# Optimization experiments

Measured on AMD Instinct MI355X. Metric: run time of the kernel, lower is better.

The kernel has to match this reference:

```python
import jax, jax.numpy as jnp
import numpy as np

N_ENTS = 100000
N_EDGES = 200000
H = 256
NUM_RELS = 200  # embedding table has 2*NUM_RELS rows
TYPE_DIM = H // 4


def layer_norm(x, g, b, eps=1e-5):
    m = jnp.mean(x, axis=-1, keepdims=True)
    v = jnp.var(x, axis=-1, keepdims=True)
    return (x - m) * jax.lax.rsqrt(v + eps) * g + b


def setup_inputs() -> dict:
    key = jax.random.key(0)
    ks = jax.random.split(key, 20)
    s = 0.02  # xavier-ish scale for weights
    return {
        "node_emb": jax.random.normal(ks[0], (N_ENTS, H), jnp.float32),
        "h_prev": jax.random.normal(ks[1], (N_ENTS, H), jnp.float32),
        "type_emb": jax.random.normal(ks[2], (2 * NUM_RELS, TYPE_DIM), jnp.float32) * s,
        "W_edge": jax.random.normal(ks[3], (2 * H + TYPE_DIM, H), jnp.float32) * s,
        "b_edge": jnp.zeros((H,), jnp.float32),
        "ln_edge_g": jnp.ones((H,), jnp.float32),
        "ln_edge_b": jnp.zeros((H,), jnp.float32),
        "W_gate": jax.random.normal(ks[4], (2 * H, H), jnp.float32) * s,
        "b_gate": jnp.zeros((H,), jnp.float32),
        "ln_gate_g": jnp.ones((H,), jnp.float32),
        "ln_gate_b": jnp.zeros((H,), jnp.float32),
        "W_ih": jax.random.normal(ks[5], (3 * H, H), jnp.float32) * s,
        "W_hh": jax.random.normal(ks[6], (3 * H, H), jnp.float32) * s,
        "b_ih": jnp.zeros((3 * H,), jnp.float32),
        "b_hh": jnp.zeros((3 * H,), jnp.float32),
        "ln_gru_g": jnp.ones((H,), jnp.float32),
        "ln_gru_b": jnp.zeros((H,), jnp.float32),
        "src": jax.random.randint(ks[7], (N_EDGES,), 0, N_ENTS, jnp.int32),
        "dst": jax.random.randint(ks[8], (N_EDGES,), 0, N_ENTS, jnp.int32),
        "edge_types": jax.random.randint(ks[9], (N_EDGES,), 0, 2 * NUM_RELS, jnp.int32),
    }


def reference(node_emb, h_prev, type_emb, W_edge, b_edge, ln_edge_g, ln_edge_b,
              W_gate, b_gate, ln_gate_g, ln_gate_b,
              W_ih, W_hh, b_ih, b_hh, ln_gru_g, ln_gru_b,
              src, dst, edge_types):
    # --- EdgeFeatureExtractor: gather + edge MLP (dropout=eval identity) ---
    edge_in = jnp.concatenate(
        [node_emb[src], node_emb[dst], type_emb[edge_types]], axis=1)  # [E, 2H+H/4]
    edge_feat = jax.nn.relu(
        layer_norm(edge_in @ W_edge + b_edge, ln_edge_g, ln_edge_b))  # [E, H]

    # --- create_edge_enhanced_nodes: scatter-mean over dst ---
    agg = jax.ops.segment_sum(edge_feat, dst, num_segments=N_ENTS)  # [N, H]
    cnt = jax.ops.segment_sum(jnp.ones((edge_feat.shape[0],), edge_feat.dtype),
                              dst, num_segments=N_ENTS)
    edge_enh = agg / jnp.clip(cnt, 1.0)[:, None]

    # --- DualStreamProcessor fusion ---
    gate = jax.nn.sigmoid(layer_norm(
        jnp.concatenate([node_emb, edge_enh], axis=1) @ W_gate + b_gate,
        ln_gate_g, ln_gate_b))
    fused = gate * node_emb + (1.0 - gate) * edge_enh
    x = 0.2 * node_emb + 0.8 * fused

    # --- EnhancedGRUCell: torch GRUCell + LayerNorm + 0.3*h residual ---
    gi = x @ W_ih.T + b_ih      # [N, 3H]
    gh = h_prev @ W_hh.T + b_hh  # [N, 3H]
    gi_r, gi_z, gi_n = jnp.split(gi, 3, axis=1)
    gh_r, gh_z, gh_n = jnp.split(gh, 3, axis=1)
    r = jax.nn.sigmoid(gi_r + gh_r)
    z = jax.nn.sigmoid(gi_z + gh_z)
    n = jnp.tanh(gi_n + r * gh_n)
    h = (1.0 - z) * n + z * h_prev
    h = layer_norm(h, ln_gru_g, ln_gru_b) + 0.3 * h_prev
    return h
```

## Files before the change

kernel.cpp:

```cpp
#include <hip/hip_runtime.h>
#include <hip/hip_bf16.h>
#include <hip/hip_fp16.h>

#define H 256
#define TYPE_DIM 64
#define EIN (2*H + TYPE_DIM)
#define N_ENTS 100000
#define N_EDGES 200000
#define EPB 32
#define NPB 64
#define KE 576
#define LDE 584
#define LDF 260
#define LDA 520
#define LDH 264
#define LDF2 260

typedef __hip_bfloat16 bf16;
typedef short bf16x8 __attribute__((ext_vector_type(8)));
typedef float f32x4 __attribute__((ext_vector_type(4)));

__device__ __forceinline__ unsigned short f2b(float f) {
    union { float f; unsigned int u; } v; v.f = f;
    unsigned int u = v.u;
    return (unsigned short)((u + 0x7FFFu + ((u >> 16) & 1u)) >> 16);
}
__device__ __forceinline__ unsigned int pack2(float a, float b) {
    return (unsigned int)f2b(a) | ((unsigned int)f2b(b) << 16);
}
__device__ __forceinline__ float u2f(unsigned short u) {
    union { unsigned int i; float f; } t; t.i = ((unsigned int)u) << 16; return t.f;
}
__device__ __forceinline__ float sigm(float x) { return 1.0f / (1.0f + __expf(-x)); }

__device__ __forceinline__ void atomic_pk_f16(void* p, unsigned int v) {
    asm volatile("global_atomic_pk_add_f16 %0, %1, off" :: "v"(p), "v"(v) : "memory");
}

__device__ __forceinline__ bf16x8 cvt8(const float* p) {
    f32x4 a = *(const f32x4*)p;
    f32x4 b = *(const f32x4*)(p + 4);
    union { bf16 h[8]; bf16x8 v; } u;
    u.h[0] = __float2bfloat16(a[0]); u.h[1] = __float2bfloat16(a[1]);
    u.h[2] = __float2bfloat16(a[2]); u.h[3] = __float2bfloat16(a[3]);
    u.h[4] = __float2bfloat16(b[0]); u.h[5] = __float2bfloat16(b[1]);
    u.h[6] = __float2bfloat16(b[2]); u.h[7] = __float2bfloat16(b[3]);
    return u.v;
}

__global__ void transpose_we(const float* __restrict__ W,
                             unsigned short* __restrict__ WE) {
    int c = blockIdx.x;
    for (int j = threadIdx.x; j < KE; j += 256)
        WE[(size_t)c * KE + j] = f2b(W[(size_t)j * H + c]);
}

__global__ void transpose_wg(const float* __restrict__ W,
                             unsigned short* __restrict__ WG) {
    int c = blockIdx.x;
    for (int k = threadIdx.x; k < 2 * H; k += 256)
        WG[(size_t)c * (2 * H) + k] = f2b(W[(size_t)k * H + c]);
}

__global__ void cast_gru(const float* __restrict__ Wih, const float* __restrict__ Whh,
                         unsigned short* __restrict__ WTih,
                         unsigned short* __restrict__ WThh, int do_hh) {
    int j = blockIdx.x;
    int k = threadIdx.x;
    WTih[(size_t)j * H + k] = f2b(Wih[(size_t)j * H + k]);
    if (do_hh) WThh[(size_t)j * H + k] = f2b(Whh[(size_t)j * H + k]);
}

__global__ __launch_bounds__(256) void edge_mfma(
    const float* __restrict__ node_emb, const float* __restrict__ type_emb,
    const unsigned short* __restrict__ WE,
    const float* __restrict__ b_edge,
    const float* __restrict__ ln_g, const float* __restrict__ ln_b,
    const int* __restrict__ src, const int* __restrict__ dst,
    const int* __restrict__ et,
    unsigned char* __restrict__ aggb,
    unsigned int* __restrict__ cntw) {
    __shared__ __align__(16) unsigned short ein[EPB * LDE];
    __shared__ int sidx[EPB], didx[EPB], tidx[EPB];

    const int tid = threadIdx.x;
    const int e0 = blockIdx.x * EPB;
    const int lane = tid & 63;
    const int w = tid >> 6;
    const int l15 = lane & 15;
    const int l4 = lane >> 4;

    if (tid < EPB) {
        sidx[tid] = src[e0 + tid];
        didx[tid] = dst[e0 + tid];
        tidx[tid] = et[e0 + tid];
    }
    __syncthreads();

    {
        const int half = tid >> 7;
        const int tt = tid & 127;
        #pragma unroll 4
        for (int e = 0; e < EPB; e++) {
            const int n = half ? didx[e] : sidx[e];
            const float2 v = *(const float2*)(node_emb + (size_t)n * H + 2 * tt);
            *(unsigned int*)&ein[e * LDE + half * 256 + 2 * tt] = pack2(v.x, v.y);
        }
        #pragma unroll
        for (int i = tid; i < EPB * 32; i += 256) {
            const int e = i >> 5, j = i & 31;
            const float2 v = *(const float2*)(type_emb + (size_t)tidx[e] * TYPE_DIM + 2 * j);
            *(unsigned int*)&ein[e * LDE + 512 + 2 * j] = pack2(v.x, v.y);
        }
    }
    __syncthreads();

    f32x4 acc[2][4];
    #pragma unroll
    for (int mt = 0; mt < 2; mt++)
        #pragma unroll
        for (int nt = 0; nt < 4; nt++)
            acc[mt][nt] = (f32x4){0.f, 0.f, 0.f, 0.f};

    const int colbase = w * 64;
    const unsigned short* A0 = &ein[l15 * LDE + l4 * 8];
    const unsigned short* A1 = &ein[(16 + l15) * LDE + l4 * 8];
    const unsigned short* B0 = WE + (size_t)(colbase + l15) * KE + l4 * 8;
    const unsigned short* B1 = B0 + 16 * KE;
    const unsigned short* B2 = B0 + 32 * KE;
    const unsigned short* B3 = B0 + 48 * KE;

    for (int ks = 0; ks < KE / 32; ks++) {
        const int o = ks * 32;
        bf16x8 a0 = __builtin_bit_cast(bf16x8, *(const uint4*)(A0 + o));
        bf16x8 a1 = __builtin_bit_cast(bf16x8, *(const uint4*)(A1 + o));
        bf16x8 b0 = __builtin_bit_cast(bf16x8, *(const uint4*)(B0 + o));
        bf16x8 b1 = __builtin_bit_cast(bf16x8, *(const uint4*)(B1 + o));
        bf16x8 b2 = __builtin_bit_cast(bf16x8, *(const uint4*)(B2 + o));
        bf16x8 b3 = __builtin_bit_cast(bf16x8, *(const uint4*)(B3 + o));
        acc[0][0] = __builtin_amdgcn_mfma_f32_16x16x32_bf16(a0, b0, acc[0][0], 0, 0, 0);
        acc[0][1] = __builtin_amdgcn_mfma_f32_16x16x32_bf16(a0, b1, acc[0][1], 0, 0, 0);
        acc[0][2] = __builtin_amdgcn_mfma_f32_16x16x32_bf16(a0, b2, acc[0][2], 0, 0, 0);
        acc[0][3] = __builtin_amdgcn_mfma_f32_16x16x32_bf16(a0, b3, acc[0][3], 0, 0, 0);
        acc[1][0] = __builtin_amdgcn_mfma_f32_16x16x32_bf16(a1, b0, acc[1][0], 0, 0, 0);
        acc[1][1] = __builtin_amdgcn_mfma_f32_16x16x32_bf16(a1, b1, acc[1][1], 0, 0, 0);
        acc[1][2] = __builtin_amdgcn_mfma_f32_16x16x32_bf16(a1, b2, acc[1][2], 0, 0, 0);
        acc[1][3] = __builtin_amdgcn_mfma_f32_16x16x32_bf16(a1, b3, acc[1][3], 0, 0, 0);
    }

    __syncthreads();
    float* fout = (float*)&ein[0];

    float bias[4];
    #pragma unroll
    for (int nt = 0; nt < 4; nt++) bias[nt] = b_edge[colbase + nt * 16 + l15];
    #pragma unroll
    for (int mt = 0; mt < 2; mt++)
        #pragma unroll
        for (int nt = 0; nt < 4; nt++)
            #pragma unroll
            for (int r = 0; r < 4; r++) {
                int row = mt * 16 + l4 * 4 + r;
                fout[row * LDF + colbase + nt * 16 + l15] = acc[mt][nt][r] + bias[nt];
            }
    __syncthreads();

    const float4 gv = *(const float4*)(ln_g + 4 * lane);
    const float4 bv = *(const float4*)(ln_b + 4 * lane);
    for (int rr = 0; rr < 8; rr++) {
        const int row = w * 8 + rr;
        f32x4 v = *(const f32x4*)&fout[row * LDF + 4 * lane];
        float s1 = v[0] + v[1] + v[2] + v[3];
        float s2 = v[0] * v[0] + v[1] * v[1] + v[2] * v[2] + v[3] * v[3];
        #pragma unroll
        for (int o = 32; o > 0; o >>= 1) {
            s1 += __shfl_down(s1, o, 64);
            s2 += __shfl_down(s2, o, 64);
        }
        const float m = __shfl(s1, 0, 64) * (1.0f / (float)H);
        const float q = __shfl(s2, 0, 64) * (1.0f / (float)H);
        const float is = rsqrtf(fmaxf(q - m * m, 0.0f) + 1e-5f);
        float y0 = fmaxf((v[0] - m) * is * gv.x + bv.x, 0.0f);
        float y1 = fmaxf((v[1] - m) * is * gv.y + bv.y, 0.0f);
        float y2 = fmaxf((v[2] - m) * is * gv.z + bv.z, 0.0f);
        float y3 = fmaxf((v[3] - m) * is * gv.w + bv.w, 0.0f);
        __half2 h01 = __floats2half2_rn(y0, y1);
        __half2 h23 = __floats2half2_rn(y2, y3);
        unsigned char* dp = aggb + (size_t)didx[row] * 1024 + lane * 8;
        atomic_pk_f16(dp,     __builtin_bit_cast(unsigned int, h01));
        atomic_pk_f16(dp + 4, __builtin_bit_cast(unsigned int, h23));
    }
    if (tid < EPB) {
        int d = didx[tid];
        atomicAdd(&cntw[d >> 2], 1u << ((d & 3) * 8));
    }
}

template<bool SHH>
__global__ __launch_bounds__(1024, 4) void node_mfma(
    const float* __restrict__ node_emb, const float* __restrict__ h_prev,
    const unsigned short* __restrict__ WG, const float* __restrict__ b_gate,
    const float* __restrict__ lng_g, const float* __restrict__ lng_b,
    const unsigned short* __restrict__ WTih, const unsigned short* __restrict__ WThh,
    const float* __restrict__ Whh_f32,
    const float* __restrict__ b_ih, const float* __restrict__ b_hh,
    const float* __restrict__ lnr_g, const float* __restrict__ lnr_b,
    const unsigned int* __restrict__ cntw,
    float* __restrict__ out) {
    __shared__ __align__(16) unsigned short Aga[NPB * LDA];
    __shared__ __align__(16) unsigned short shr[NPB * LDH];
    __shared__ float rc[NPB];

    const int tid = threadIdx.x;
    const int n0 = blockIdx.x * NPB;
    const int lane = tid & 63;
    const int w = tid >> 6;
    const int l15 = lane & 15, l4 = lane >> 4;

    if (tid < NPB) {
        int n = n0 + tid;
        float c = 1.0f;
        if (n < N_ENTS) {
            unsigned int cw = cntw[n >> 2];
            c = (float)((cw >> ((n & 3) * 8)) & 0xFFu);
        }
        rc[tid] = 1.0f / fmaxf(c, 1.0f);
    }
    __syncthreads();

    const unsigned char* aggb = (const unsigned char*)out;

    for (int i = tid; i < NPB * 128; i += 1024) {
        int row = i >> 7, c2 = (i & 127) * 2;
        int nr = n0 + row;
        size_t gn = (size_t)(nr < N_ENTS ? nr : 0);
        float2 xv = *(const float2*)(node_emb + gn * H + c2);
        unsigned int eu = *(const unsigned int*)(aggb + gn * 1024 + c2 * 2);
        float2 ev = __half22float2(__builtin_bit_cast(__half2, eu));
        float r = rc[row];
        *(unsigned int*)&Aga[row * LDA + c2]       = pack2(xv.x, xv.y);
        *(unsigned int*)&Aga[row * LDA + 256 + c2] = pack2(ev.x * r, ev.y * r);
    }
    __syncthreads();

    {
        f32x4 acc[4];
        #pragma unroll
        for (int m = 0; m < 4; m++) acc[m] = (f32x4){0.f, 0.f, 0.f, 0.f};
        const unsigned short* Ab = &Aga[l15 * LDA + l4 * 8];
        const unsigned short* B0 = WG + (size_t)(w * 16 + l15) * (2 * H) + l4 * 8;
        #pragma unroll 4
        for (int ks = 0; ks < 16; ks++) {
            const int o = ks * 32;
            bf16x8 b0 = __builtin_bit_cast(bf16x8, *(const uint4*)(B0 + o));
            #pragma unroll
            for (int m = 0; m < 4; m++) {
                bf16x8 a = __builtin_bit_cast(bf16x8, *(const uint4*)(Ab + m * 16 * LDA + o));
                acc[m] = __builtin_amdgcn_mfma_f32_16x16x32_bf16(a, b0, acc[m], 0, 0, 0);
            }
        }
        const float bg0 = b_gate[w * 16 + l15];
        #pragma unroll
        for (int m = 0; m < 4; m++)
            #pragma unroll
            for (int r = 0; r < 4; r++) {
                int row = m * 16 + l4 * 4 + r;
                shr[row * LDH + w * 16 + l15] = f2b(acc[m][r] + bg0);
            }
    }
    __syncthreads();

    {
        const float4 g4 = *(const float4*)(lng_g + 4 * lane);
        const float4 b4 = *(const float4*)(lng_b + 4 * lane);
        for (int rr = 0; rr < 4; rr++) {
            const int row = w * 4 + rr;
            short4 us = *(const short4*)&shr[row * LDH + 4 * lane];
            float u0 = u2f((unsigned short)us.x), u1 = u2f((unsigned short)us.y);
            float u2 = u2f((unsigned short)us.z), u3 = u2f((unsigned short)us.w);
            float s1 = u0 + u1 + u2 + u3;
            float s2 = u0 * u0 + u1 * u1 + u2 * u2 + u3 * u3;
            #pragma unroll
            for (int o = 32; o > 0; o >>= 1) {
                s1 += __shfl_down(s1, o, 64);
                s2 += __shfl_down(s2, o, 64);
            }
            const float m = __shfl(s1, 0, 64) * (1.0f / (float)H);
            const float q = __shfl(s2, 0, 64) * (1.0f / (float)H);
            const float is = rsqrtf(fmaxf(q - m * m, 0.0f) + 1e-5f);
            short4 xr = *(const short4*)&Aga[row * LDA + 4 * lane];
            short4 er = *(const short4*)&Aga[row * LDA + 256 + 4 * lane];
            float xv[4] = {u2f((unsigned short)xr.x), u2f((unsigned short)xr.y),
                           u2f((unsigned short)xr.z), u2f((unsigned short)xr.w)};
            float ev[4] = {u2f((unsigned short)er.x), u2f((unsigned short)er.y),
                           u2f((unsigned short)er.z), u2f((unsigned short)er.w)};
            float uu[4] = {u0, u1, u2, u3};
            float gl[4] = {g4.x, g4.y, g4.z, g4.w};
            float bl[4] = {b4.x, b4.y, b4.z, b4.w};
            unsigned short xs[4];
            #pragma unroll
            for (int j = 0; j < 4; j++) {
                float gate = sigm((uu[j] - m) * is * gl[j] + bl[j]);
                float fused = gate * xv[j] + (1.0f - gate) * ev[j];
                xs[j] = f2b(0.2f * xv[j] + 0.8f * fused);
            }
            *(unsigned int*)&Aga[row * LDA + 4 * lane]     = (unsigned int)xs[0] | ((unsigned int)xs[1] << 16);
            *(unsigned int*)&Aga[row * LDA + 4 * lane + 2] = (unsigned int)xs[2] | ((unsigned int)xs[3] << 16);
        }
    }
    __syncthreads();

    for (int i = tid; i < NPB * 128; i += 1024) {
        int row = i >> 7, c2 = (i & 127) * 2;
        int nr = n0 + row;
        size_t g = (size_t)(nr < N_ENTS ? nr : 0) * H + c2;
        float2 hv = *(const float2*)(h_prev + g);
        *(unsigned int*)&shr[row * LDH + c2] = pack2(hv.x, hv.y);
    }
    __syncthreads();

    const int cl = w * 16 + l15;
    const unsigned short* Xb = &Aga[l15 * LDA + l4 * 8];
    const unsigned short* Pb = &shr[l15 * LDH + l4 * 8];

    float rg[4][4], zg[4][4];
    {
        f32x4 aIr[4], aIz[4], aHr[4], aHz[4];
        #pragma unroll
        for (int m = 0; m < 4; m++) {
            aIr[m] = (f32x4){0.f, 0.f, 0.f, 0.f}; aIz[m] = (f32x4){0.f, 0.f, 0.f, 0.f};
            aHr[m] = (f32x4){0.f, 0.f, 0.f, 0.f}; aHz[m] = (f32x4){0.f, 0.f, 0.f, 0.f};
        }
        const unsigned short* bi0 = WTih + (size_t)(cl) * H + l4 * 8;
        const unsigned short* bi1 = WTih + (size_t)(H + cl) * H + l4 * 8;
        const unsigned short* bh0s = WThh + (size_t)(cl) * H + l4 * 8;
        const unsigned short* bh1s = WThh + (size_t)(H + cl) * H + l4 * 8;
        const float* fh0 = Whh_f32 + (size_t)(cl) * H + l4 * 8;
        const float* fh1 = Whh_f32 + (size_t)(H + cl) * H + l4 * 8;
        #pragma unroll 4
        for (int ks = 0; ks < 8; ks++) {
            const int o = ks * 32;
            bf16x8 vI0 = __builtin_bit_cast(bf16x8, *(const uint4*)(bi0 + o));
            bf16x8 vI1 = __builtin_bit_cast(bf16x8, *(const uint4*)(bi1 + o));
            bf16x8 vH0, vH1;
            if (SHH) {
                vH0 = __builtin_bit_cast(bf16x8, *(const uint4*)(bh0s + o));
                vH1 = __builtin_bit_cast(bf16x8, *(const uint4*)(bh1s + o));
            } else {
                vH0 = cvt8(fh0 + o);
                vH1 = cvt8(fh1 + o);
            }
            #pragma unroll
            for (int m = 0; m < 4; m++) {
                bf16x8 ax = __builtin_bit_cast(bf16x8, *(const uint4*)(Xb + m * 16 * LDA + o));
                bf16x8 ah = __builtin_bit_cast(bf16x8, *(const uint4*)(Pb + m * 16 * LDH + o));
                aIr[m] = __builtin_amdgcn_mfma_f32_16x16x32_bf16(ax, vI0, aIr[m], 0, 0, 0);
                aIz[m] = __builtin_amdgcn_mfma_f32_16x16x32_bf16(ax, vI1, aIz[m], 0, 0, 0);
                aHr[m] = __builtin_amdgcn_mfma_f32_16x16x32_bf16(ah, vH0, aHr[m], 0, 0, 0);
                aHz[m] = __builtin_amdgcn_mfma_f32_16x16x32_bf16(ah, vH1, aHz[m], 0, 0, 0);
            }
        }
        const float bi_0 = b_ih[cl], bi_1 = b_ih[H + cl];
        const float bh_0 = b_hh[cl], bh_1 = b_hh[H + cl];
        #pragma unroll
        for (int m = 0; m < 4; m++)
            #pragma unroll
            for (int r = 0; r < 4; r++) {
                rg[m][r] = sigm(aIr[m][r] + bi_0 + aHr[m][r] + bh_0);
                zg[m][r] = sigm(aIz[m][r] + bi_1 + aHz[m][r] + bh_1);
            }
    }

    float hreg[4][4];
    {
        f32x4 aIn[4], aHn[4];
        #pragma unroll
        for (int m = 0; m < 4; m++) {
            aIn[m] = (f32x4){0.f, 0.f, 0.f, 0.f};
            aHn[m] = (f32x4){0.f, 0.f, 0.f, 0.f};
        }
        const unsigned short* bi2 = WTih + (size_t)(2 * H + cl) * H + l4 * 8;
        const unsigned short* bh2s = WThh + (size_t)(2 * H + cl) * H + l4 * 8;
        const float* fh2 = Whh_f32 + (size_t)(2 * H + cl) * H + l4 * 8;
        #pragma unroll 4
        for (int ks = 0; ks < 8; ks++) {
            const int o = ks * 32;
            bf16x8 vI2 = __builtin_bit_cast(bf16x8, *(const uint4*)(bi2 + o));
            bf16x8 vH2;
            if (SHH) vH2 = __builtin_bit_cast(bf16x8, *(const uint4*)(bh2s + o));
            else     vH2 = cvt8(fh2 + o);
            #pragma unroll
            for (int m = 0; m < 4; m++) {
                bf16x8 ax = __builtin_bit_cast(bf16x8, *(const uint4*)(Xb + m * 16 * LDA + o));
                bf16x8 ah = __builtin_bit_cast(bf16x8, *(const uint4*)(Pb + m * 16 * LDH + o));
                aIn[m] = __builtin_amdgcn_mfma_f32_16x16x32_bf16(ax, vI2, aIn[m], 0, 0, 0);
                aHn[m] = __builtin_amdgcn_mfma_f32_16x16x32_bf16(ah, vH2, aHn[m], 0, 0, 0);
            }
        }
        const float bi_2 = b_ih[2 * H + cl];
        const float bh_2 = b_hh[2 * H + cl];
        #pragma unroll
        for (int m = 0; m < 4; m++)
            #pragma unroll
            for (int r = 0; r < 4; r++) {
                const int row = m * 16 + l4 * 4 + r;
                int nr = n0 + row; if (nr >= N_ENTS) nr = N_ENTS - 1;
                float nn = tanhf(aIn[m][r] + bi_2 + rg[m][r] * (aHn[m][r] + bh_2));
                float hpv = h_prev[(size_t)nr * H + cl];
                hreg[m][r] = (1.0f - zg[m][r]) * nn + zg[m][r] * hpv;
            }
    }
    __syncthreads();

    float* hb = (float*)&Aga[0];
    #pragma unroll
    for (int m = 0; m < 4; m++)
        #pragma unroll
        for (int r = 0; r < 4; r++)
            hb[(m * 16 + l4 * 4 + r) * LDF2 + cl] = hreg[m][r];
    __syncthreads();

    {
        const float4 g4 = *(const float4*)(lnr_g + 4 * lane);
        const float4 b4 = *(const float4*)(lnr_b + 4 * lane);
        for (int rr = 0; rr < 4; rr++) {
            const int row = w * 4 + rr;
            const int nr = n0 + row;
            f32x4 hv = *(const f32x4*)&hb[row * LDF2 + 4 * lane];
            float s1 = hv[0] + hv[1] + hv[2] + hv[3];
            float s2 = hv[0] * hv[0] + hv[1] * hv[1] + hv[2] * hv[2] + hv[3] * hv[3];
            #pragma unroll
            for (int o = 32; o > 0; o >>= 1) {
                s1 += __shfl_down(s1, o, 64);
                s2 += __shfl_down(s2, o, 64);
            }
            const float m = __shfl(s1, 0, 64) * (1.0f / (float)H);
            const float q = __shfl(s2, 0, 64) * (1.0f / (float)H);
            const float is = rsqrtf(fmaxf(q - m * m, 0.0f) + 1e-5f);
            if (nr < N_ENTS) {
                const float4 hp4 = *(const float4*)(h_prev + (size_t)nr * H + 4 * lane);
                float4 o4;
                o4.x = (hv[0] - m) * is * g4.x + b4.x + 0.3f * hp4.x;
                o4.y = (hv[1] - m) * is * g4.y + b4.y + 0.3f * hp4.y;
                o4.z = (hv[2] - m) * is * g4.z + b4.z + 0.3f * hp4.z;
                o4.w = (hv[3] - m) * is * g4.w + b4.w + 0.3f * hp4.w;
                *(float4*)(out + (size_t)nr * H + 4 * lane) = o4;
            }
        }
    }
}

extern "C" void kernel_launch(void* const* d_in, const int* in_sizes, int n_in,
                              void* d_out, int out_size, void* d_ws, size_t ws_size,
                              hipStream_t stream) {
    (void)in_sizes; (void)n_in; (void)out_size;
    const float* node_emb  = (const float*)d_in[0];
    const float* h_prev    = (const float*)d_in[1];
    const float* type_emb  = (const float*)d_in[2];
    const float* W_edge    = (const float*)d_in[3];
    const float* b_edge    = (const float*)d_in[4];
    const float* ln_edge_g = (const float*)d_in[5];
    const float* ln_edge_b = (const float*)d_in[6];
    const float* W_gate    = (const float*)d_in[7];
    const float* b_gate    = (const float*)d_in[8];
    const float* ln_gate_g = (const float*)d_in[9];
    const float* ln_gate_b = (const float*)d_in[10];
    const float* W_ih      = (const float*)d_in[11];
    const float* W_hh      = (const float*)d_in[12];
    const float* b_ih      = (const float*)d_in[13];
    const float* b_hh      = (const float*)d_in[14];
    const float* ln_gru_g  = (const float*)d_in[15];
    const float* ln_gru_b  = (const float*)d_in[16];
    const int*   src       = (const int*)d_in[17];
    const int*   dst       = (const int*)d_in[18];
    const int*   et        = (const int*)d_in[19];
    float* out = (float*)d_out;

    char* ws = (char*)d_ws;
    unsigned int* cntw  = (unsigned int*)ws;
    unsigned short* WE   = (unsigned short*)(ws + 100000);
    unsigned short* WG   = (unsigned short*)(ws + 100000);
    unsigned short* WTih = (unsigned short*)(ws + 362144);
    unsigned short* WThh = (unsigned short*)(ws + 755360);
    const bool big = ws_size >= (size_t)1148576;

    hipMemsetAsync(cntw, 0, 100000, stream);
    hipMemsetAsync(out, 0, (size_t)N_ENTS * H * sizeof(float), stream);

    hipLaunchKernelGGL(transpose_we, dim3(256), dim3(256), 0, stream, W_edge, WE);

    hipLaunchKernelGGL(edge_mfma, dim3(N_EDGES / EPB), dim3(256), 0, stream,
                       node_emb, type_emb, WE, b_edge, ln_edge_g, ln_edge_b,
                       src, dst, et, (unsigned char*)out, cntw);

    hipLaunchKernelGGL(transpose_wg, dim3(256), dim3(256), 0, stream, W_gate, WG);
    hipLaunchKernelGGL(cast_gru, dim3(768), dim3(256), 0, stream,
                       W_ih, W_hh, WTih, WThh, big ? 1 : 0);

    const int nblocks = (N_ENTS + NPB - 1) / NPB;
    if (big) {
        hipLaunchKernelGGL((node_mfma<true>), dim3(nblocks), dim3(1024), 0, stream,
                           node_emb, h_prev, WG, b_gate, ln_gate_g, ln_gate_b,
                           WTih, WThh, W_hh, b_ih, b_hh, ln_gru_g, ln_gru_b,
                           cntw, out);
    } else {
        hipLaunchKernelGGL((node_mfma<false>), dim3(nblocks), dim3(1024), 0, stream,
                           node_emb, h_prev, WG, b_gate, ln_gate_g, ln_gate_b,
                           WTih, WTih , W_hh, b_ih, b_hh, ln_gru_g, ln_gru_b,
                           cntw, out);
    }
}
```

Measured before the change: 990.3 us.

## Swizzle node kernel LDS layout, prefetch h_prev early, merge GRU r/z accumulators

Replaces the padded shared-memory row strides in the node kernel with unpadded rows and an XOR swizzle on the 16-byte column chunk, aimed at avoiding LDS bank conflicts and shrinking LDS use. It also widens the staging loads to float4, prefetches h_prev into registers before the gate GEMM so the global latency overlaps compute, and folds the input and hidden r/z matmuls into a single accumulator each, cutting register pressure. The swizzle has to stay consistent across every read and write site, and that includes the fp32 reuse of the buffer.

```diff
diff --git a/kernel.cpp b/kernel.cpp
--- a/kernel.cpp
+++ b/kernel.cpp
@@ -12,9 +12,6 @@
 #define KE 576
 #define LDE 584
 #define LDF 260
-#define LDA 520
-#define LDH 264
-#define LDF2 260
 
 typedef __hip_bfloat16 bf16;
 typedef short bf16x8 __attribute__((ext_vector_type(8)));
@@ -46,6 +43,11 @@
     u.h[4] = __float2bfloat16(b[0]); u.h[5] = __float2bfloat16(b[1]);
     u.h[6] = __float2bfloat16(b[2]); u.h[7] = __float2bfloat16(b[3]);
     return u.v;
+}
+
+__device__ __forceinline__ bf16x8 ldsA(const char* base, int row, int kbyte, int stride) {
+    return __builtin_bit_cast(bf16x8,
+        *(const uint4*)(base + (((row * stride) + kbyte) ^ ((row & 7) << 4))));
 }
 
 __global__ void transpose_we(const float* __restrict__ W,
@@ -207,8 +209,8 @@
     const float* __restrict__ lnr_g, const float* __restrict__ lnr_b,
     const unsigned int* __restrict__ cntw,
     float* __restrict__ out) {
-    __shared__ __align__(16) unsigned short Aga[NPB * LDA];
-    __shared__ __align__(16) unsigned short shr[NPB * LDH];
+    __shared__ __align__(16) unsigned short Aga[NPB * 512];
+    __shared__ __align__(16) unsigned short shr[NPB * 256];
     __shared__ float rc[NPB];
 
     const int tid = threadIdx.x;
@@ -216,6 +218,8 @@
     const int lane = tid & 63;
     const int w = tid >> 6;
     const int l15 = lane & 15, l4 = lane >> 4;
+    char* AgaB = (char*)Aga;
+    char* shrB = (char*)shr;
 
     if (tid < NPB) {
         int n = n0 + tid;
@@ -230,16 +234,32 @@
 
     const unsigned char* aggb = (const unsigned char*)out;
 
-    for (int i = tid; i < NPB * 128; i += 1024) {
-        int row = i >> 7, c2 = (i & 127) * 2;
+    #pragma unroll
+    for (int j = 0; j < 4; j++) {
+        int i = tid + j * 1024;
+        int row = i >> 6, c4 = (i & 63) * 4;
         int nr = n0 + row;
         size_t gn = (size_t)(nr < N_ENTS ? nr : 0);
-        float2 xv = *(const float2*)(node_emb + gn * H + c2);
-        unsigned int eu = *(const unsigned int*)(aggb + gn * 1024 + c2 * 2);
-        float2 ev = __half22float2(__builtin_bit_cast(__half2, eu));
+        float4 xv = *(const float4*)(node_emb + gn * H + c4);
+        uint2 eu = *(const uint2*)(aggb + gn * 1024 + c4 * 2);
+        float2 e01 = __half22float2(__builtin_bit_cast(__half2, eu.x));
+        float2 e23 = __half22float2(__builtin_bit_cast(__half2, eu.y));
         float r = rc[row];
-        *(unsigned int*)&Aga[row * LDA + c2]       = pack2(xv.x, xv.y);
-        *(unsigned int*)&Aga[row * LDA + 256 + c2] = pack2(ev.x * r, ev.y * r);
+        int swz = (row & 7) << 4;
+        uint2 xp, ep;
+        xp.x = pack2(xv.x, xv.y); xp.y = pack2(xv.z, xv.w);
+        ep.x = pack2(e01.x * r, e01.y * r); ep.y = pack2(e23.x * r, e23.y * r);
+        *(uint2*)(AgaB + ((row * 1024 + c4 * 2) ^ swz)) = xp;
+        *(uint2*)(AgaB + ((row * 1024 + 512 + c4 * 2) ^ swz)) = ep;
+    }
+
+    float4 hpre[4];
+    #pragma unroll
+    for (int j = 0; j < 4; j++) {
+        int i = tid + j * 1024;
+        int row = i >> 6, c4 = (i & 63) * 4;
+        int nr = n0 + row;
+        hpre[j] = *(const float4*)(h_prev + (size_t)(nr < N_ENTS ? nr : 0) * H + c4);
     }
     __syncthreads();
 
@@ -247,15 +267,14 @@
         f32x4 acc[4];
         #pragma unroll
         for (int m = 0; m < 4; m++) acc[m] = (f32x4){0.f, 0.f, 0.f, 0.f};
-        const unsigned short* Ab = &Aga[l15 * LDA + l4 * 8];
         const unsigned short* B0 = WG + (size_t)(w * 16 + l15) * (2 * H) + l4 * 8;
         #pragma unroll 4
         for (int ks = 0; ks < 16; ks++) {
-            const int o = ks * 32;
-            bf16x8 b0 = __builtin_bit_cast(bf16x8, *(const uint4*)(B0 + o));
+            bf16x8 b0 = __builtin_bit_cast(bf16x8, *(const uint4*)(B0 + ks * 32));
+            const int kb = ks * 64 + l4 * 16;
             #pragma unroll
             for (int m = 0; m < 4; m++) {
-                bf16x8 a = __builtin_bit_cast(bf16x8, *(const uint4*)(Ab + m * 16 * LDA + o));
+                bf16x8 a = ldsA(AgaB, m * 16 + l15, kb, 1024);
                 acc[m] = __builtin_amdgcn_mfma_f32_16x16x32_bf16(a, b0, acc[m], 0, 0, 0);
             }
         }
@@ -265,7 +284,8 @@
             #pragma unroll
             for (int r = 0; r < 4; r++) {
                 int row = m * 16 + l4 * 4 + r;
-                shr[row * LDH + w * 16 + l15] = f2b(acc[m][r] + bg0);
+                *(unsigned short*)(shrB + ((row * 512 + (w * 16 + l15) * 2) ^ ((row & 7) << 4)))
+                    = f2b(acc[m][r] + bg0);
             }
     }
     __syncthreads();
@@ -275,7 +295,8 @@
         const float4 b4 = *(const float4*)(lng_b + 4 * lane);
         for (int rr = 0; rr < 4; rr++) {
             const int row = w * 4 + rr;
-            short4 us = *(const short4*)&shr[row * LDH + 4 * lane];
+            const int swz = (row & 7) << 4;
+            short4 us = *(const short4*)(shrB + ((row * 512 + lane * 8) ^ swz));
             float u0 = u2f((unsigned short)us.x), u1 = u2f((unsigned short)us.y);
             float u2 = u2f((unsigned short)us.z), u3 = u2f((unsigned short)us.w);
             float s1 = u0 + u1 + u2 + u3;
@@ -288,8 +309,8 @@
             const float m = __shfl(s1, 0, 64) * (1.0f / (float)H);
             const float q = __shfl(s2, 0, 64) * (1.0f / (float)H);
             const float is = rsqrtf(fmaxf(q - m * m, 0.0f) + 1e-5f);
-            short4 xr = *(const short4*)&Aga[row * LDA + 4 * lane];
-            short4 er = *(const short4*)&Aga[row * LDA + 256 + 4 * lane];
+            short4 xr = *(const short4*)(AgaB + ((row * 1024 + lane * 8) ^ swz));
+            short4 er = *(const short4*)(AgaB + ((row * 1024 + 512 + lane * 8) ^ swz));
             float xv[4] = {u2f((unsigned short)xr.x), u2f((unsigned short)xr.y),
                            u2f((unsigned short)xr.z), u2f((unsigned short)xr.w)};
             float ev[4] = {u2f((unsigned short)er.x), u2f((unsigned short)er.y),
@@ -304,32 +325,35 @@
                 float fused = gate * xv[j] + (1.0f - gate) * ev[j];
                 xs[j] = f2b(0.2f * xv[j] + 0.8f * fused);
             }
-            *(unsigned int*)&Aga[row * LDA + 4 * lane]     = (unsigned int)xs[0] | ((unsigned int)xs[1] << 16);
-            *(unsigned int*)&Aga[row * LDA + 4 * lane + 2] = (unsigned int)xs[2] | ((unsigned int)xs[3] << 16);
-        }
-    }
-    __syncthreads();
-
-    for (int i = tid; i < NPB * 128; i += 1024) {
-        int row = i >> 7, c2 = (i & 127) * 2;
-        int nr = n0 + row;
-        size_t g = (size_t)(nr < N_ENTS ? nr : 0) * H + c2;
-        float2 hv = *(const float2*)(h_prev + g);
-        *(unsigned int*)&shr[row * LDH + c2] = pack2(hv.x, hv.y);
+            uint2 xp;
+            xp.x = (unsigned int)xs[0] | ((unsigned int)xs[1] << 16);
+            xp.y = (unsigned int)xs[2] | ((unsigned int)xs[3] << 16);
+            *(uint2*)(AgaB + ((row * 1024 + lane * 8) ^ swz)) = xp;
+        }
+    }
+    __syncthreads();
+
+    #pragma unroll
+    for (int j = 0; j < 4; j++) {
+        int i = tid + j * 1024;
+        int row = i >> 6, c4 = (i & 63) * 4;
+        int swz = (row & 7) << 4;
+        uint2 hp2;
+        hp2.x = pack2(hpre[j].x, hpre[j].y);
+        hp2.y = pack2(hpre[j].z, hpre[j].w);
+        *(uint2*)(shrB + ((row * 512 + c4 * 2) ^ swz)) = hp2;
     }
     __syncthreads();
 
     const int cl = w * 16 + l15;
-    const unsigned short* Xb = &Aga[l15 * LDA + l4 * 8];
-    const unsigned short* Pb = &shr[l15 * LDH + l4 * 8];
 
     float rg[4][4], zg[4][4];
     {
-        f32x4 aIr[4], aIz[4], aHr[4], aHz[4];
+        f32x4 ar[4], az[4];
         #pragma unroll
         for (int m = 0; m < 4; m++) {
-            aIr[m] = (f32x4){0.f, 0.f, 0.f, 0.f}; aIz[m] = (f32x4){0.f, 0.f, 0.f, 0.f};
-            aHr[m] = (f32x4){0.f, 0.f, 0.f, 0.f}; aHz[m] = (f32x4){0.f, 0.f, 0.f, 0.f};
+            ar[m] = (f32x4){0.f, 0.f, 0.f, 0.f};
+            az[m] = (f32x4){0.f, 0.f, 0.f, 0.f};
         }
         const unsigned short* bi0 = WTih + (size_t)(cl) * H + l4 * 8;
         const unsigned short* bi1 = WTih + (size_t)(H + cl) * H + l4 * 8;
@@ -340,6 +364,7 @@
         #pragma unroll 4
         for (int ks = 0; ks < 8; ks++) {
             const int o = ks * 32;
+            const int kb = ks * 64 + l4 * 16;
             bf16x8 vI0 = __builtin_bit_cast(bf16x8, *(const uint4*)(bi0 + o));
             bf16x8 vI1 = __builtin_bit_cast(bf16x8, *(const uint4*)(bi1 + o));
             bf16x8 vH0, vH1;
@@ -352,12 +377,13 @@
             }
             #pragma unroll
             for (int m = 0; m < 4; m++) {
-                bf16x8 ax = __builtin_bit_cast(bf16x8, *(const uint4*)(Xb + m * 16 * LDA + o));
-                bf16x8 ah = __builtin_bit_cast(bf16x8, *(const uint4*)(Pb + m * 16 * LDH + o));
-                aIr[m] = __builtin_amdgcn_mfma_f32_16x16x32_bf16(ax, vI0, aIr[m], 0, 0, 0);
-                aIz[m] = __builtin_amdgcn_mfma_f32_16x16x32_bf16(ax, vI1, aIz[m], 0, 0, 0);
-                aHr[m] = __builtin_amdgcn_mfma_f32_16x16x32_bf16(ah, vH0, aHr[m], 0, 0, 0);
-                aHz[m] = __builtin_amdgcn_mfma_f32_16x16x32_bf16(ah, vH1, aHz[m], 0, 0, 0);
+                const int rw = m * 16 + l15;
+                bf16x8 ax = ldsA(AgaB, rw, kb, 1024);
+                bf16x8 ah = ldsA(shrB, rw, kb, 512);
+                ar[m] = __builtin_amdgcn_mfma_f32_16x16x32_bf16(ax, vI0, ar[m], 0, 0, 0);
+                ar[m] = __builtin_amdgcn_mfma_f32_16x16x32_bf16(ah, vH0, ar[m], 0, 0, 0);
+                az[m] = __builtin_amdgcn_mfma_f32_16x16x32_bf16(ax, vI1, az[m], 0, 0, 0);
+                az[m] = __builtin_amdgcn_mfma_f32_16x16x32_bf16(ah, vH1, az[m], 0, 0, 0);
             }
         }
         const float bi_0 = b_ih[cl], bi_1 = b_ih[H + cl];
@@ -366,8 +392,8 @@
         for (int m = 0; m < 4; m++)
             #pragma unroll
             for (int r = 0; r < 4; r++) {
-                rg[m][r] = sigm(aIr[m][r] + bi_0 + aHr[m][r] + bh_0);
-                zg[m][r] = sigm(aIz[m][r] + bi_1 + aHz[m][r] + bh_1);
+                rg[m][r] = sigm(ar[m][r] + bi_0 + bh_0);
+                zg[m][r] = sigm(az[m][r] + bi_1 + bh_1);
             }
     }
 
@@ -385,14 +411,16 @@
         #pragma unroll 4
         for (int ks = 0; ks < 8; ks++) {
             const int o = ks * 32;
+            const int kb = ks * 64 + l4 * 16;
             bf16x8 vI2 = __builtin_bit_cast(bf16x8, *(const uint4*)(bi2 + o));
             bf16x8 vH2;
             if (SHH) vH2 = __builtin_bit_cast(bf16x8, *(const uint4*)(bh2s + o));
             else     vH2 = cvt8(fh2 + o);
             #pragma unroll
             for (int m = 0; m < 4; m++) {
-                bf16x8 ax = __builtin_bit_cast(bf16x8, *(const uint4*)(Xb + m * 16 * LDA + o));
-                bf16x8 ah = __builtin_bit_cast(bf16x8, *(const uint4*)(Pb + m * 16 * LDH + o));
+                const int rw = m * 16 + l15;
+                bf16x8 ax = ldsA(AgaB, rw, kb, 1024);
+                bf16x8 ah = ldsA(shrB, rw, kb, 512);
                 aIn[m] = __builtin_amdgcn_mfma_f32_16x16x32_bf16(ax, vI2, aIn[m], 0, 0, 0);
                 aHn[m] = __builtin_amdgcn_mfma_f32_16x16x32_bf16(ah, vH2, aHn[m], 0, 0, 0);
             }
@@ -413,11 +441,14 @@
     __syncthreads();
 
     float* hb = (float*)&Aga[0];
+    (void)hb;
     #pragma unroll
     for (int m = 0; m < 4; m++)
         #pragma unroll
-        for (int r = 0; r < 4; r++)
-            hb[(m * 16 + l4 * 4 + r) * LDF2 + cl] = hreg[m][r];
+        for (int r = 0; r < 4; r++) {
+            const int row = m * 16 + l4 * 4 + r;
+            *(float*)(AgaB + ((row * 1024 + cl * 4) ^ ((row & 7) << 4))) = hreg[m][r];
+        }
     __syncthreads();
 
     {
@@ -426,7 +457,7 @@
         for (int rr = 0; rr < 4; rr++) {
             const int row = w * 4 + rr;
             const int nr = n0 + row;
-            f32x4 hv = *(const f32x4*)&hb[row * LDF2 + 4 * lane];
+            f32x4 hv = *(const f32x4*)(AgaB + ((row * 1024 + lane * 16) ^ ((row & 7) << 4)));
             float s1 = hv[0] + hv[1] + hv[2] + hv[3];
             float s2 = hv[0] * hv[0] + hv[1] * hv[1] + hv[2] * hv[2] + hv[3] * hv[3];
             #pragma unroll
```

Result: faster. 968.3 us (-2.2%).
